# Optimization experiments

Measured on AMD Instinct MI355X. Metric: run time of the kernel, lower is better.

## Reference

```python
import jax, jax.numpy as jnp
import numpy as np

B, T, U = 4, 256, 128
EH, PH, JH, V = 1024, 640, 640, 1024


def setup_inputs() -> dict:
    key = jax.random.key(0)
    ks = jax.random.split(key, 8)
    s_e = 1.0 / np.sqrt(EH)
    s_p = 1.0 / np.sqrt(PH)
    s_j = 1.0 / np.sqrt(JH)
    return {
        "enc": jax.random.normal(ks[0], (B, EH, T), jnp.float32),
        "dec": jax.random.normal(ks[1], (B, PH, U), jnp.float32),
        "W_enc": jax.random.uniform(ks[2], (JH, EH), jnp.float32, -s_e, s_e),
        "b_enc": jax.random.uniform(ks[3], (JH,), jnp.float32, -s_e, s_e),
        "W_pred": jax.random.uniform(ks[4], (JH, PH), jnp.float32, -s_p, s_p),
        "b_pred": jax.random.uniform(ks[5], (JH,), jnp.float32, -s_p, s_p),
        "W_out": jax.random.uniform(ks[6], (V, JH), jnp.float32, -s_j, s_j),
        "b_out": jax.random.uniform(ks[7], (V,), jnp.float32, -s_j, s_j),
    }


def reference(enc, dec, W_enc, b_enc, W_pred, b_pred, W_out, b_out):
    # enc: [B, EH, T], dec: [B, PH, U]  (channels-first, as in torch forward)
    # enc projection -> [B, T, JH] (transpose fused into einsum)
    e = jnp.einsum('bht,jh->btj', enc, W_enc) + b_enc
    # pred projection -> [B, U, JH]
    p = jnp.einsum('bhu,jh->buj', dec, W_pred) + b_pred
    # broadcast add -> [B, T, U, JH], ReLU, output projection -> [B, T, U, V]
    h = jax.nn.relu(e[:, :, None, :] + p[:, None, :, :])
    logits = jnp.einsum('btuj,vj->btuv', h, W_out) + b_out
    return jax.nn.log_softmax(logits, axis=-1)
```

## Files before the change

### kernel.cpp

```cpp
#include <hip/hip_runtime.h>
#include <hip/hip_bf16.h>
#include <stdint.h>

#define B_ 4
#define T_ 256
#define U_ 128
#define EH_ 1024
#define PH_ 640
#define JH_ 640
#define V_ 1024
#define KT_ 20

typedef short bf16x8 __attribute__((ext_vector_type(8)));
typedef float f32x4 __attribute__((ext_vector_type(4)));
typedef unsigned short u16;

__device__ __forceinline__ u16 f2bf(float f) {
  union { float f; uint32_t u; } v;
  v.f = f;
  uint32_t u = v.u;
  return (u16)((u + 0x7FFFu + ((u >> 16) & 1u)) >> 16);
}

__device__ __forceinline__ uint32_t cvt2(float lo, float hi) {
  uint32_t r;
  asm("v_cvt_pk_bf16_f32 %0, %1, %2" : "=v"(r) : "v"(lo), "v"(hi));
  return r;
}

#define LGKM0  asm volatile("s_waitcnt lgkmcnt(0)" ::: "memory")

__global__ void k_transpose_cvt(const float* __restrict__ in, u16* __restrict__ out,
                                int H, int W) {
  __shared__ float tile[32][33];
  int b = blockIdx.z;
  int h0 = blockIdx.y * 32, w0 = blockIdx.x * 32;
  const float* pin = in + (size_t)b * H * W;
  u16* pout = out + (size_t)b * H * W;
  int lw = threadIdx.x & 31, lh = threadIdx.x >> 5;
#pragma unroll
  for (int i = 0; i < 4; i++) {
    int h = lh + i * 8;
    tile[h][lw] = pin[(size_t)(h0 + h) * W + (w0 + lw)];
  }
  __syncthreads();
#pragma unroll
  for (int i = 0; i < 4; i++) {
    int w = lh + i * 8;
    pout[(size_t)(w0 + w) * H + (h0 + lw)] = f2bf(tile[lw][w]);
  }
}

__global__ void k_prep_w(const float* __restrict__ We, const float* __restrict__ Wp,
                         const float* __restrict__ Wo,
                         u16* __restrict__ WeB, u16* __restrict__ WpB,
                         u16* __restrict__ Wpk) {
  int s = blockIdx.x * 256 + threadIdx.x;
  if (s < 163840) {
    int idx = s * 4;
    float4 v = *(const float4*)(We + idx);
    ushort4 o;
    o.x = f2bf(v.x); o.y = f2bf(v.y); o.z = f2bf(v.z); o.w = f2bf(v.w);
    *(ushort4*)(WeB + idx) = o;
  } else if (s < 266240) {
    int idx = (s - 163840) * 4;
    float4 v = *(const float4*)(Wp + idx);
    ushort4 o;
    o.x = f2bf(v.x); o.y = f2bf(v.y); o.z = f2bf(v.z); o.w = f2bf(v.w);
    *(ushort4*)(WpB + idx) = o;
  } else {
    int q = s - 266240;
    int c = q & 1023;
    int g = (q >> 10) & 3;
    int t = q >> 12;
    const float* src = Wo + (size_t)c * JH_ + t * 32 + g * 8;
    float4 a = *(const float4*)src;
    float4 b2 = *(const float4*)(src + 4);
    ushort4 lo, hi;
    lo.x = f2bf(a.x);  lo.y = f2bf(a.y);  lo.z = f2bf(a.z);  lo.w = f2bf(a.w);
    hi.x = f2bf(b2.x); hi.y = f2bf(b2.y); hi.z = f2bf(b2.z); hi.w = f2bf(b2.w);
    u16* d = Wpk + (size_t)q * 8;
    *(ushort4*)d = lo;
    *(ushort4*)(d + 4) = hi;
  }
}

__global__ void k_proj_gemm(const u16* __restrict__ A, const u16* __restrict__ Bm,
                            const float* __restrict__ bias, float* __restrict__ C,
                            int K, int N, size_t strideA, size_t strideC) {
  __shared__ __align__(16) u16 sA[64 * 64];
  __shared__ __align__(16) u16 sB[64 * 64];
  int bb = blockIdx.z;
  const u16* Ab = A + (size_t)bb * strideA;
  float* Cb = C + (size_t)bb * strideC;
  int m0 = blockIdx.x * 64, n0 = blockIdx.y * 64;
  int tid = threadIdx.x;
  int lane = tid & 63, wid = tid >> 6;

  f32x4 acc[2][2] = {};
  for (int kk = 0; kk < K; kk += 64) {
#pragma unroll
    for (int i = 0; i < 2; i++) {
      int c = tid + i * 256;
      int r = c >> 3, kc = c & 7;
      int s = (r << 3) | (kc ^ (r & 7));
      *(bf16x8*)(sA + s * 8) = *(const bf16x8*)(Ab + (size_t)(m0 + r) * K + kk + kc * 8);
      *(bf16x8*)(sB + s * 8) = *(const bf16x8*)(Bm + (size_t)(n0 + r) * K + kk + kc * 8);
    }
    __syncthreads();
    int wr = (wid >> 1) * 32, wc = (wid & 1) * 32;
    int lr = lane & 15, lk = lane >> 4;
#pragma unroll
    for (int ki = 0; ki < 2; ki++) {
      bf16x8 af[2], bq[2];
#pragma unroll
      for (int mf = 0; mf < 2; mf++) {
        int r = wr + mf * 16 + lr;
        int kc = ki * 4 + lk;
        int s = (r << 3) | (kc ^ (r & 7));
        af[mf] = *(const bf16x8*)(sA + s * 8);
      }
#pragma unroll
      for (int nf = 0; nf < 2; nf++) {
        int r = wc + nf * 16 + lr;
        int kc = ki * 4 + lk;
        int s = (r << 3) | (kc ^ (r & 7));
        bq[nf] = *(const bf16x8*)(sB + s * 8);
      }
#pragma unroll
      for (int mf = 0; mf < 2; mf++)
#pragma unroll
        for (int nf = 0; nf < 2; nf++)
          acc[mf][nf] = __builtin_amdgcn_mfma_f32_16x16x32_bf16(af[mf], bq[nf], acc[mf][nf], 0, 0, 0);
    }
    __syncthreads();
  }
  int wr = (wid >> 1) * 32, wc = (wid & 1) * 32;
  int lr = lane & 15, lq = lane >> 4;
#pragma unroll
  for (int nf = 0; nf < 2; nf++) {
    int n = n0 + wc + nf * 16 + lr;
    float bv = bias[n];
#pragma unroll
    for (int mf = 0; mf < 2; mf++) {
#pragma unroll
      for (int r = 0; r < 4; r++) {
        int m = m0 + wr + mf * 16 + lq * 4 + r;
        Cb[(size_t)m * N + n] = acc[mf][nf][r] + bv;
      }
    }
  }
}

__global__ void k_pack_p2(const float* __restrict__ pBuf, float* __restrict__ pPk) {
  int s = blockIdx.x * 256 + threadIdx.x;
  int bh = s / 10240;
  int rem = s - bh * 10240;
  int g4 = rem >> 6;
  int r = rem & 63;
  int b = bh >> 1, half = bh & 1;
  const float* src = pBuf + ((size_t)(b * 128 + half * 64 + r)) * JH_ + g4 * 4;
  float4 v = *(const float4*)src;
  *(float4*)(pPk + (size_t)s * 4) = v;
}

__global__ __launch_bounds__(512)
void k_fused4(const float* __restrict__ e, const float* __restrict__ pPk,
              const u16* __restrict__ Wpk, const float* __restrict__ bout,
              float* __restrict__ out) {
  __shared__ __align__(16) u16 sA[2][4096];
  __shared__ __align__(16) float sE[JH_];
  __shared__ float redm[512];
  __shared__ float reds[512];

  int bid = blockIdx.x;
  int btile = bid >> 1, half = bid & 1, b = btile >> 8;
  int tid = threadIdx.x, lane = tid & 63, wn = tid >> 6;
  int lr = lane & 15, lk = lane >> 4;
  int ph = (bid % 10) * 2;

  const float* eRow = e + (size_t)btile * JH_;
  const float* pPbase = pPk + ((size_t)(b * 2 + half) * 40960) + wn * 256 + lane * 4;
  const u16* wB = Wpk + ((size_t)lk * 1024 + wn * 128 + lr) * 8;
  float* outB = out + ((size_t)btile * U_ + half * 64) * V_;

  int awr = (wn >> 1) * 512 + lane * 8 + (wn & 1) * 4;

  f32x4 acc[4][8] = {};
  bf16x8 bq[2][8];

  auto tp = [&](int t) { int x = t + ph; return x >= KT_ ? x - KT_ : x; };
  auto loadB = [&](int tph, bf16x8* d) {
#pragma unroll
    for (int nf = 0; nf < 8; nf++)
      d[nf] = *(const bf16x8*)(wB + (size_t)tph * 32768 + nf * 128);
  };
  auto loadp = [&](int tph) { return *(const float4*)(pPbase + tph * 2048); };
  auto build = [&](int slot, int tin, int tph, float4 pv) {
    float4 ev = *(const float4*)(&sE[tph * 32 + wn * 4]);
    uint2 w;
    w.x = cvt2(fmaxf(pv.x + ev.x, 0.f), fmaxf(pv.y + ev.y, 0.f));
    w.y = cvt2(fmaxf(pv.z + ev.z, 0.f), fmaxf(pv.w + ev.w, 0.f));
    *(uint2*)(&sA[slot][tin * 2048 + awr]) = w;
  };

  loadB(tp(0), bq[0]);
  for (int i = tid; i < JH_; i += 512) sE[i] = eRow[i];
  float4 p0  = loadp(tp(0));
  float4 p1  = loadp(tp(1));
  float4 pcA = loadp(tp(2));
  float4 pcB = loadp(tp(3));
  float4 pnA = p0, pnB = p0;
  LGKM0;
  __builtin_amdgcn_s_barrier();
  build(0, 0, tp(0), p0);
  build(0, 1, tp(1), p1);
  LGKM0;
  __builtin_amdgcn_s_barrier();

#pragma unroll
  for (int t = 0; t < KT_; t++) {
    if (t + 1 < KT_) loadB(tp(t + 1), bq[(t + 1) & 1]);
    if ((t & 1) == 0) {
      if (t + 4 < KT_) { pnA = loadp(tp(t + 4)); pnB = loadp(tp(t + 5)); }
      if (t + 2 < KT_) {
        int q1 = ((t >> 1) + 1) & 1;
        build(q1, 0, tp(t + 2), pcA);
        build(q1, 1, tp(t + 3), pcB);
      }
    }
    const u16* Ab = &sA[(t >> 1) & 1][(t & 1) * 2048 + lk * 512];
    bf16x8 af[4];
#pragma unroll
    for (int mf = 0; mf < 4; mf++)
      af[mf] = *(const bf16x8*)(Ab + (mf * 16 + lr) * 8);
    __builtin_amdgcn_s_setprio(1);
#pragma unroll
    for (int mf = 0; mf < 4; mf++)
#pragma unroll
      for (int nf = 0; nf < 8; nf++)
        acc[mf][nf] = __builtin_amdgcn_mfma_f32_16x16x32_bf16(af[mf], bq[t & 1][nf], acc[mf][nf], 0, 0, 0);
    __builtin_amdgcn_s_setprio(0);
    if ((t & 1) && t + 1 < KT_) {
      pcA = pnA; pcB = pnB;
      LGKM0;
      __builtin_amdgcn_s_barrier();
    }
  }

  float bv[8];
#pragma unroll
  for (int nf = 0; nf < 8; nf++) bv[nf] = bout[wn * 128 + nf * 16 + lr];
#pragma unroll
  for (int mf = 0; mf < 4; mf++)
#pragma unroll
    for (int nf = 0; nf < 8; nf++)
#pragma unroll
      for (int r = 0; r < 4; r++)
        acc[mf][nf][r] += bv[nf];

  float gm[4][4];
#pragma unroll
  for (int mf = 0; mf < 4; mf++)
#pragma unroll
    for (int r = 0; r < 4; r++) {
      float m = acc[mf][0][r];
#pragma unroll
      for (int nf = 1; nf < 8; nf++) m = fmaxf(m, acc[mf][nf][r]);
#pragma unroll
      for (int o = 1; o < 16; o <<= 1) m = fmaxf(m, __shfl_xor(m, o, 64));
      gm[mf][r] = m;
    }
  if ((lane & 15) == 0) {
#pragma unroll
    for (int mf = 0; mf < 4; mf++)
#pragma unroll
      for (int r = 0; r < 4; r++)
        redm[(mf * 16 + lk * 4 + r) * 8 + wn] = gm[mf][r];
  }
  __syncthreads();
#pragma unroll
  for (int mf = 0; mf < 4; mf++)
#pragma unroll
    for (int r = 0; r < 4; r++) {
      int row = mf * 16 + lk * 4 + r;
      float m = redm[row * 8];
#pragma unroll
      for (int w = 1; w < 8; w++) m = fmaxf(m, redm[row * 8 + w]);
      gm[mf][r] = m;
    }
  float ls[4][4];
#pragma unroll
  for (int mf = 0; mf < 4; mf++)
#pragma unroll
    for (int r = 0; r < 4; r++) {
      float s = 0.f;
#pragma unroll
      for (int nf = 0; nf < 8; nf++) s += __expf(acc[mf][nf][r] - gm[mf][r]);
#pragma unroll
      for (int o = 1; o < 16; o <<= 1) s += __shfl_xor(s, o, 64);
      ls[mf][r] = s;
    }
  if ((lane & 15) == 0) {
#pragma unroll
    for (int mf = 0; mf < 4; mf++)
#pragma unroll
      for (int r = 0; r < 4; r++)
        reds[(mf * 16 + lk * 4 + r) * 8 + wn] = ls[mf][r];
  }
  __syncthreads();
#pragma unroll
  for (int mf = 0; mf < 4; mf++)
#pragma unroll
    for (int r = 0; r < 4; r++) {
      int row = mf * 16 + lk * 4 + r;
      float s = reds[row * 8];
#pragma unroll
      for (int w = 1; w < 8; w++) s += reds[row * 8 + w];
      ls[mf][r] = gm[mf][r] + __logf(s);
    }
#pragma unroll
  for (int mf = 0; mf < 4; mf++)
#pragma unroll
    for (int nf = 0; nf < 8; nf++)
#pragma unroll
      for (int r = 0; r < 4; r++)
        outB[(size_t)(mf * 16 + lk * 4 + r) * V_ + wn * 128 + nf * 16 + lr] =
            acc[mf][nf][r] - ls[mf][r];
}

extern "C" void kernel_launch(void* const* d_in, const int* in_sizes, int n_in,
                              void* d_out, int out_size, void* d_ws, size_t ws_size,
                              hipStream_t stream) {
  const float* enc    = (const float*)d_in[0];
  const float* dec    = (const float*)d_in[1];
  const float* W_enc  = (const float*)d_in[2];
  const float* b_enc  = (const float*)d_in[3];
  const float* W_pred = (const float*)d_in[4];
  const float* b_pred = (const float*)d_in[5];
  const float* W_out  = (const float*)d_in[6];
  const float* b_out  = (const float*)d_in[7];
  float* out = (float*)d_out;

  char* ws = (char*)d_ws;
  size_t off = 0;
  auto alloc = [&](size_t bytes) {
    void* pp = ws + off;
    off = (off + bytes + 255) & ~(size_t)255;
    return pp;
  };
  u16* encT   = (u16*)alloc((size_t)B_ * T_ * EH_ * 2);
  u16* decT   = (u16*)alloc((size_t)B_ * U_ * PH_ * 2);
  u16* WencB  = (u16*)alloc((size_t)JH_ * EH_ * 2);
  u16* WpredB = (u16*)alloc((size_t)JH_ * PH_ * 2);
  u16* Wpk    = (u16*)alloc((size_t)KT_ * 32768 * 2);
  float* eBuf = (float*)alloc((size_t)B_ * T_ * JH_ * 4);
  float* pBuf = (float*)alloc((size_t)B_ * U_ * JH_ * 4);
  float* pPk  = (float*)alloc((size_t)81920 * 4 * 4);

  k_transpose_cvt<<<dim3(T_ / 32, EH_ / 32, B_), 256, 0, stream>>>(enc, encT, EH_, T_);
  k_transpose_cvt<<<dim3(U_ / 32, PH_ / 32, B_), 256, 0, stream>>>(dec, decT, PH_, U_);
  k_prep_w<<<1360, 256, 0, stream>>>(W_enc, W_pred, W_out, WencB, WpredB, Wpk);
  k_proj_gemm<<<dim3(T_ / 64, JH_ / 64, B_), 256, 0, stream>>>(
      encT, WencB, b_enc, eBuf, EH_, JH_, (size_t)T_ * EH_, (size_t)T_ * JH_);
  k_proj_gemm<<<dim3(U_ / 64, JH_ / 64, B_), 256, 0, stream>>>(
      decT, WpredB, b_pred, pBuf, PH_, JH_, (size_t)U_ * PH_, (size_t)U_ * JH_);
  k_pack_p2<<<320, 256, 0, stream>>>(pBuf, pPk);

  k_fused4<<<B_ * T_ * 2, 512, 0, stream>>>(eBuf, pPk, Wpk, b_out, out);
}
```

Baseline: 298.9 us.

## Stage full pred tile in LDS as bf16 and build A fragments per wave

The fused joint kernel now loads the whole 64x640 pred slice into LDS as bf16 once at block start. Each wave then builds its own A fragments in registers (add enc row, ReLU, convert to bf16) from LDS, instead of cooperatively building a double-buffered shared A tile with a barrier every two k-steps. Per-wave k-phase staggering and launch bounds of two blocks per CU aim to cut barrier stalls and spread weight-load traffic. In exchange, each wave redoes the ReLU/convert work, LDS use grows to about 83 KB, and the pred values are rounded to bf16 before the add.

```diff
diff --git a/kernel.cpp b/kernel.cpp
--- a/kernel.cpp
+++ b/kernel.cpp
@@ -13,6 +13,7 @@
 
 typedef short bf16x8 __attribute__((ext_vector_type(8)));
 typedef float f32x4 __attribute__((ext_vector_type(4)));
+typedef uint32_t u32x4 __attribute__((ext_vector_type(4)));
 typedef unsigned short u16;
 
 __device__ __forceinline__ u16 f2bf(float f) {
@@ -28,7 +29,11 @@
   return r;
 }
 
-#define LGKM0  asm volatile("s_waitcnt lgkmcnt(0)" ::: "memory")
+__device__ __forceinline__ float asf(uint32_t u) {
+  union { uint32_t u; float f; } v;
+  v.u = u;
+  return v.f;
+}
 
 __global__ void k_transpose_cvt(const float* __restrict__ in, u16* __restrict__ out,
                                 int H, int W) {
@@ -164,11 +169,11 @@
   *(float4*)(pPk + (size_t)s * 4) = v;
 }
 
-__global__ __launch_bounds__(512)
-void k_fused4(const float* __restrict__ e, const float* __restrict__ pPk,
+__global__ __launch_bounds__(512, 2)
+void k_fused5(const float* __restrict__ e, const float* __restrict__ pPk,
               const u16* __restrict__ Wpk, const float* __restrict__ bout,
               float* __restrict__ out) {
-  __shared__ __align__(16) u16 sA[2][4096];
+  __shared__ __align__(16) u16 sP[64 * 648];
   __shared__ __align__(16) float sE[JH_];
   __shared__ float redm[512];
   __shared__ float reds[512];
@@ -177,75 +182,81 @@
   int btile = bid >> 1, half = bid & 1, b = btile >> 8;
   int tid = threadIdx.x, lane = tid & 63, wn = tid >> 6;
   int lr = lane & 15, lk = lane >> 4;
-  int ph = (bid % 10) * 2;
+  int phw = ((bid >> 3) * 7 + wn * 2) % KT_;
 
   const float* eRow = e + (size_t)btile * JH_;
-  const float* pPbase = pPk + ((size_t)(b * 2 + half) * 40960) + wn * 256 + lane * 4;
+  const float* pPbase = pPk + ((size_t)(b * 2 + half) * 40960);
   const u16* wB = Wpk + ((size_t)lk * 1024 + wn * 128 + lr) * 8;
   float* outB = out + ((size_t)btile * U_ + half * 64) * V_;
 
-  int awr = (wn >> 1) * 512 + lane * 8 + (wn & 1) * 4;
+  for (int i = tid; i < JH_; i += 512) sE[i] = eRow[i];
+#pragma unroll
+  for (int i = 0; i < 20; i++) {
+    int s = i * 512 + tid;
+    int r = s & 63, g4 = s >> 6;
+    float4 v = *(const float4*)(pPbase + (size_t)s * 4);
+    uint2 w2;
+    w2.x = cvt2(v.x, v.y);
+    w2.y = cvt2(v.z, v.w);
+    *(uint2*)(&sP[r * 648 + g4 * 4]) = w2;
+  }
+  __syncthreads();
 
   f32x4 acc[4][8] = {};
   bf16x8 bq[2][8];
-
-  auto tp = [&](int t) { int x = t + ph; return x >= KT_ ? x - KT_ : x; };
-  auto loadB = [&](int tph, bf16x8* d) {
+  u32x4 pd[2][4];
+  f32x4 ev[2][2];
+  bf16x8 af[4];
+
+  auto tpw = [&](int t) { int x = t + phw; return x >= KT_ ? x - KT_ : x; };
+  auto loadB = [&](int tw, bf16x8* d) {
 #pragma unroll
     for (int nf = 0; nf < 8; nf++)
-      d[nf] = *(const bf16x8*)(wB + (size_t)tph * 32768 + nf * 128);
+      d[nf] = *(const bf16x8*)(wB + (size_t)tw * 32768 + nf * 128);
   };
-  auto loadp = [&](int tph) { return *(const float4*)(pPbase + tph * 2048); };
-  auto build = [&](int slot, int tin, int tph, float4 pv) {
-    float4 ev = *(const float4*)(&sE[tph * 32 + wn * 4]);
-    uint2 w;
-    w.x = cvt2(fmaxf(pv.x + ev.x, 0.f), fmaxf(pv.y + ev.y, 0.f));
-    w.y = cvt2(fmaxf(pv.z + ev.z, 0.f), fmaxf(pv.w + ev.w, 0.f));
-    *(uint2*)(&sA[slot][tin * 2048 + awr]) = w;
+  auto loadA = [&](int tw, u32x4* pdv, f32x4* evv) {
+    int ko = tw * 32 + lk * 8;
+#pragma unroll
+    for (int mf = 0; mf < 4; mf++)
+      pdv[mf] = *(const u32x4*)(&sP[(mf * 16 + lr) * 648 + ko]);
+    evv[0] = *(const f32x4*)(&sE[ko]);
+    evv[1] = *(const f32x4*)(&sE[ko + 4]);
   };
-
-  loadB(tp(0), bq[0]);
-  for (int i = tid; i < JH_; i += 512) sE[i] = eRow[i];
-  float4 p0  = loadp(tp(0));
-  float4 p1  = loadp(tp(1));
-  float4 pcA = loadp(tp(2));
-  float4 pcB = loadp(tp(3));
-  float4 pnA = p0, pnB = p0;
-  LGKM0;
-  __builtin_amdgcn_s_barrier();
-  build(0, 0, tp(0), p0);
-  build(0, 1, tp(1), p1);
-  LGKM0;
-  __builtin_amdgcn_s_barrier();
+  auto build = [&](const u32x4* pdv, const f32x4* evv) {
+#pragma unroll
+    for (int mf = 0; mf < 4; mf++) {
+      union { uint32_t u[4]; bf16x8 v; } r;
+#pragma unroll
+      for (int j = 0; j < 4; j++) {
+        uint32_t u = pdv[mf][j];
+        float lo = asf(u << 16);
+        float hi = asf(u & 0xffff0000u);
+        float el = evv[j >> 1][(j & 1) * 2];
+        float eh = evv[j >> 1][(j & 1) * 2 + 1];
+        r.u[j] = cvt2(fmaxf(lo + el, 0.f), fmaxf(hi + eh, 0.f));
+      }
+      af[mf] = r.v;
+    }
+  };
+
+  loadA(tpw(0), pd[0], ev[0]);
+  loadB(tpw(0), bq[0]);
 
 #pragma unroll
   for (int t = 0; t < KT_; t++) {
-    if (t + 1 < KT_) loadB(tp(t + 1), bq[(t + 1) & 1]);
-    if ((t & 1) == 0) {
-      if (t + 4 < KT_) { pnA = loadp(tp(t + 4)); pnB = loadp(tp(t + 5)); }
-      if (t + 2 < KT_) {
-        int q1 = ((t >> 1) + 1) & 1;
-        build(q1, 0, tp(t + 2), pcA);
-        build(q1, 1, tp(t + 3), pcB);
-      }
-    }
-    const u16* Ab = &sA[(t >> 1) & 1][(t & 1) * 2048 + lk * 512];
-    bf16x8 af[4];
+    const int c = t & 1;
+    if (t + 1 < KT_) {
+      loadA(tpw(t + 1), pd[c ^ 1], ev[c ^ 1]);
+      loadB(tpw(t + 1), bq[c ^ 1]);
+    }
+    build(pd[c], ev[c]);
+    __builtin_amdgcn_s_setprio(1);
 #pragma unroll
     for (int mf = 0; mf < 4; mf++)
-      af[mf] = *(const bf16x8*)(Ab + (mf * 16 + lr) * 8);
-    __builtin_amdgcn_s_setprio(1);
-#pragma unroll
-    for (int mf = 0; mf < 4; mf++)
 #pragma unroll
       for (int nf = 0; nf < 8; nf++)
-        acc[mf][nf] = __builtin_amdgcn_mfma_f32_16x16x32_bf16(af[mf], bq[t & 1][nf], acc[mf][nf], 0, 0, 0);
+        acc[mf][nf] = __builtin_amdgcn_mfma_f32_16x16x32_bf16(af[mf], bq[c][nf], acc[mf][nf], 0, 0, 0);
     __builtin_amdgcn_s_setprio(0);
-    if ((t & 1) && t + 1 < KT_) {
-      pcA = pnA; pcB = pnB;
-      LGKM0;
-      __builtin_amdgcn_s_barrier();
-    }
   }
 
   float bv[8];
@@ -367,5 +378,5 @@
       decT, WpredB, b_pred, pBuf, PH_, JH_, (size_t)U_ * PH_, (size_t)U_ * JH_);
   k_pack_p2<<<320, 256, 0, stream>>>(pBuf, pPk);
 
-  k_fused4<<<B_ * T_ * 2, 512, 0, stream>>>(eBuf, pPk, Wpk, b_out, out);
-}
+  k_fused5<<<B_ * T_ * 2, 512, 0, stream>>>(eBuf, pPk, Wpk, b_out, out);
+}
```

Result: slower. 329.3 us (+10.2%).

## Make fused joint kernel persistent and transpose MFMA operands for vector stores

Applied to the files above, without the earlier changes.

Launches 256 persistent blocks, each looping over 8 (t, half) units instead of one block per unit, and prefetches the next unit's e row, W and p fragments while the current unit's output is written. Swaps the MFMA operand order so each lane holds four consecutive vocabulary columns. This allows 16-byte vectorized output stores and bias loads, and cuts the softmax shuffle reductions to two steps per row. The cost is fewer resident blocks, so latency hiding depends on the in-block prefetch. The sE overwrite in stageUnit also relies on barrier ordering being correct.

```diff
diff --git a/kernel.cpp b/kernel.cpp
--- a/kernel.cpp
+++ b/kernel.cpp
@@ -165,7 +165,7 @@
 }
 
 __global__ __launch_bounds__(512)
-void k_fused4(const float* __restrict__ e, const float* __restrict__ pPk,
+void k_fused6(const float* __restrict__ e, const float* __restrict__ pPk,
               const u16* __restrict__ Wpk, const float* __restrict__ bout,
               float* __restrict__ out) {
   __shared__ __align__(16) u16 sA[2][4096];
@@ -174,20 +174,17 @@
   __shared__ float reds[512];
 
   int bid = blockIdx.x;
-  int btile = bid >> 1, half = bid & 1, b = btile >> 8;
   int tid = threadIdx.x, lane = tid & 63, wn = tid >> 6;
   int lr = lane & 15, lk = lane >> 4;
   int ph = (bid % 10) * 2;
 
-  const float* eRow = e + (size_t)btile * JH_;
-  const float* pPbase = pPk + ((size_t)(b * 2 + half) * 40960) + wn * 256 + lane * 4;
   const u16* wB = Wpk + ((size_t)lk * 1024 + wn * 128 + lr) * 8;
-  float* outB = out + ((size_t)btile * U_ + half * 64) * V_;
-
   int awr = (wn >> 1) * 512 + lane * 8 + (wn & 1) * 4;
 
-  f32x4 acc[4][8] = {};
   bf16x8 bq[2][8];
+  float4 p0, p1, pcA, pcB, pnA, pnB;
+  const float* pPbase = pPk;
+  float* outB = out;
 
   auto tp = [&](int t) { int x = t + ph; return x >= KT_ ? x - KT_ : x; };
   auto loadB = [&](int tph, bf16x8* d) {
@@ -203,130 +200,128 @@
     w.y = cvt2(fmaxf(pv.z + ev.z, 0.f), fmaxf(pv.w + ev.w, 0.f));
     *(uint2*)(&sA[slot][tin * 2048 + awr]) = w;
   };
-
-  loadB(tp(0), bq[0]);
-  for (int i = tid; i < JH_; i += 512) sE[i] = eRow[i];
-  float4 p0  = loadp(tp(0));
-  float4 p1  = loadp(tp(1));
-  float4 pcA = loadp(tp(2));
-  float4 pcB = loadp(tp(3));
-  float4 pnA = p0, pnB = p0;
-  LGKM0;
-  __builtin_amdgcn_s_barrier();
-  build(0, 0, tp(0), p0);
-  build(0, 1, tp(1), p1);
-  LGKM0;
-  __builtin_amdgcn_s_barrier();
-
-#pragma unroll
-  for (int t = 0; t < KT_; t++) {
-    if (t + 1 < KT_) loadB(tp(t + 1), bq[(t + 1) & 1]);
-    if ((t & 1) == 0) {
-      if (t + 4 < KT_) { pnA = loadp(tp(t + 4)); pnB = loadp(tp(t + 5)); }
-      if (t + 2 < KT_) {
-        int q1 = ((t >> 1) + 1) & 1;
-        build(q1, 0, tp(t + 2), pcA);
-        build(q1, 1, tp(t + 3), pcB);
-      }
-    }
-    const u16* Ab = &sA[(t >> 1) & 1][(t & 1) * 2048 + lk * 512];
-    bf16x8 af[4];
-#pragma unroll
-    for (int mf = 0; mf < 4; mf++)
-      af[mf] = *(const bf16x8*)(Ab + (mf * 16 + lr) * 8);
-    __builtin_amdgcn_s_setprio(1);
-#pragma unroll
-    for (int mf = 0; mf < 4; mf++)
+  auto stageUnit = [&](int unit) {
+    int btile = unit >> 1, half = unit & 1, b = btile >> 8;
+    const float* eRow = e + (size_t)btile * JH_;
+    pPbase = pPk + ((size_t)(b * 2 + half) * 40960) + wn * 256 + lane * 4;
+    outB = out + ((size_t)btile * U_ + half * 64) * V_;
+    for (int i = tid; i < JH_; i += 512) sE[i] = eRow[i];
+    loadB(tp(0), bq[0]);
+    p0  = loadp(tp(0));
+    p1  = loadp(tp(1));
+    pcA = loadp(tp(2));
+    pcB = loadp(tp(3));
+  };
+
+  stageUnit(bid);
+
+#pragma unroll 1
+  for (int u = 0; u < 8; u++) {
+    LGKM0;
+    __builtin_amdgcn_s_barrier();
+    build(0, 0, tp(0), p0);
+    build(0, 1, tp(1), p1);
+    LGKM0;
+    __builtin_amdgcn_s_barrier();
+
+    f32x4 acc[4][8] = {};
+#pragma unroll
+    for (int t = 0; t < KT_; t++) {
+      if (t + 1 < KT_) loadB(tp(t + 1), bq[(t + 1) & 1]);
+      if ((t & 1) == 0) {
+        if (t + 4 < KT_) { pnA = loadp(tp(t + 4)); pnB = loadp(tp(t + 5)); }
+        if (t + 2 < KT_) {
+          int q1 = ((t >> 1) + 1) & 1;
+          build(q1, 0, tp(t + 2), pcA);
+          build(q1, 1, tp(t + 3), pcB);
+        }
+      }
+      const u16* Ab = &sA[(t >> 1) & 1][(t & 1) * 2048 + lk * 512];
+      bf16x8 af[4];
+#pragma unroll
+      for (int mf = 0; mf < 4; mf++)
+        af[mf] = *(const bf16x8*)(Ab + (mf * 16 + lr) * 8);
+      __builtin_amdgcn_s_setprio(1);
+#pragma unroll
+      for (int mf = 0; mf < 4; mf++)
+#pragma unroll
+        for (int nf = 0; nf < 8; nf++)
+          acc[mf][nf] = __builtin_amdgcn_mfma_f32_16x16x32_bf16(bq[t & 1][nf], af[mf], acc[mf][nf], 0, 0, 0);
+      __builtin_amdgcn_s_setprio(0);
+      if ((t & 1) && t + 1 < KT_) {
+        pcA = pnA; pcB = pnB;
+        LGKM0;
+        __builtin_amdgcn_s_barrier();
+      }
+    }
+
+#pragma unroll
+    for (int nf = 0; nf < 8; nf++) {
+      f32x4 bv = *(const f32x4*)(bout + wn * 128 + nf * 16 + lk * 4);
+#pragma unroll
+      for (int mf = 0; mf < 4; mf++) acc[mf][nf] += bv;
+    }
+    float gm[4], lsv[4];
+#pragma unroll
+    for (int mf = 0; mf < 4; mf++) {
+      float m = acc[mf][0][0];
 #pragma unroll
       for (int nf = 0; nf < 8; nf++)
-        acc[mf][nf] = __builtin_amdgcn_mfma_f32_16x16x32_bf16(af[mf], bq[t & 1][nf], acc[mf][nf], 0, 0, 0);
-    __builtin_amdgcn_s_setprio(0);
-    if ((t & 1) && t + 1 < KT_) {
-      pcA = pnA; pcB = pnB;
-      LGKM0;
-      __builtin_amdgcn_s_barrier();
-    }
-  }
-
-  float bv[8];
-#pragma unroll
-  for (int nf = 0; nf < 8; nf++) bv[nf] = bout[wn * 128 + nf * 16 + lr];
-#pragma unroll
-  for (int mf = 0; mf < 4; mf++)
-#pragma unroll
-    for (int nf = 0; nf < 8; nf++)
-#pragma unroll
-      for (int r = 0; r < 4; r++)
-        acc[mf][nf][r] += bv[nf];
-
-  float gm[4][4];
-#pragma unroll
-  for (int mf = 0; mf < 4; mf++)
-#pragma unroll
-    for (int r = 0; r < 4; r++) {
-      float m = acc[mf][0][r];
-#pragma unroll
-      for (int nf = 1; nf < 8; nf++) m = fmaxf(m, acc[mf][nf][r]);
-#pragma unroll
-      for (int o = 1; o < 16; o <<= 1) m = fmaxf(m, __shfl_xor(m, o, 64));
-      gm[mf][r] = m;
-    }
-  if ((lane & 15) == 0) {
-#pragma unroll
-    for (int mf = 0; mf < 4; mf++)
-#pragma unroll
-      for (int r = 0; r < 4; r++)
-        redm[(mf * 16 + lk * 4 + r) * 8 + wn] = gm[mf][r];
-  }
-  __syncthreads();
-#pragma unroll
-  for (int mf = 0; mf < 4; mf++)
-#pragma unroll
-    for (int r = 0; r < 4; r++) {
-      int row = mf * 16 + lk * 4 + r;
-      float m = redm[row * 8];
-#pragma unroll
-      for (int w = 1; w < 8; w++) m = fmaxf(m, redm[row * 8 + w]);
-      gm[mf][r] = m;
-    }
-  float ls[4][4];
-#pragma unroll
-  for (int mf = 0; mf < 4; mf++)
-#pragma unroll
-    for (int r = 0; r < 4; r++) {
+#pragma unroll
+        for (int j = 0; j < 4; j++) m = fmaxf(m, acc[mf][nf][j]);
+      m = fmaxf(m, __shfl_xor(m, 16, 64));
+      m = fmaxf(m, __shfl_xor(m, 32, 64));
+      gm[mf] = m;
+    }
+    if (lane < 16) {
+#pragma unroll
+      for (int mf = 0; mf < 4; mf++) redm[(mf * 16 + lr) * 8 + wn] = gm[mf];
+    }
+    __syncthreads();
+#pragma unroll
+    for (int mf = 0; mf < 4; mf++) {
+      float m = redm[(mf * 16 + lr) * 8];
+#pragma unroll
+      for (int w = 1; w < 8; w++) m = fmaxf(m, redm[(mf * 16 + lr) * 8 + w]);
+      gm[mf] = m;
+    }
+#pragma unroll
+    for (int mf = 0; mf < 4; mf++) {
       float s = 0.f;
 #pragma unroll
-      for (int nf = 0; nf < 8; nf++) s += __expf(acc[mf][nf][r] - gm[mf][r]);
-#pragma unroll
-      for (int o = 1; o < 16; o <<= 1) s += __shfl_xor(s, o, 64);
-      ls[mf][r] = s;
-    }
-  if ((lane & 15) == 0) {
-#pragma unroll
-    for (int mf = 0; mf < 4; mf++)
-#pragma unroll
-      for (int r = 0; r < 4; r++)
-        reds[(mf * 16 + lk * 4 + r) * 8 + wn] = ls[mf][r];
-  }
-  __syncthreads();
-#pragma unroll
-  for (int mf = 0; mf < 4; mf++)
-#pragma unroll
-    for (int r = 0; r < 4; r++) {
-      int row = mf * 16 + lk * 4 + r;
-      float s = reds[row * 8];
-#pragma unroll
-      for (int w = 1; w < 8; w++) s += reds[row * 8 + w];
-      ls[mf][r] = gm[mf][r] + __logf(s);
-    }
-#pragma unroll
-  for (int mf = 0; mf < 4; mf++)
-#pragma unroll
-    for (int nf = 0; nf < 8; nf++)
-#pragma unroll
-      for (int r = 0; r < 4; r++)
-        outB[(size_t)(mf * 16 + lk * 4 + r) * V_ + wn * 128 + nf * 16 + lr] =
-            acc[mf][nf][r] - ls[mf][r];
+      for (int nf = 0; nf < 8; nf++)
+#pragma unroll
+        for (int j = 0; j < 4; j++) s += __expf(acc[mf][nf][j] - gm[mf]);
+      s += __shfl_xor(s, 16, 64);
+      s += __shfl_xor(s, 32, 64);
+      lsv[mf] = s;
+    }
+    if (lane < 16) {
+#pragma unroll
+      for (int mf = 0; mf < 4; mf++) reds[(mf * 16 + lr) * 8 + wn] = lsv[mf];
+    }
+    __syncthreads();
+#pragma unroll
+    for (int mf = 0; mf < 4; mf++) {
+      float s = reds[(mf * 16 + lr) * 8];
+#pragma unroll
+      for (int w = 1; w < 8; w++) s += reds[(mf * 16 + lr) * 8 + w];
+      lsv[mf] = gm[mf] + __logf(s);
+    }
+
+    float* outC = outB;
+    if (u < 7) stageUnit((u + 1) * 256 + bid);
+
+#pragma unroll
+    for (int mf = 0; mf < 4; mf++) {
+      float* orow = outC + (size_t)(mf * 16 + lr) * V_ + wn * 128 + lk * 4;
+#pragma unroll
+      for (int nf = 0; nf < 8; nf++) {
+        f32x4 v = acc[mf][nf] - lsv[mf];
+        *(f32x4*)(orow + nf * 16) = v;
+      }
+    }
+  }
 }
 
 extern "C" void kernel_launch(void* const* d_in, const int* in_sizes, int n_in,
@@ -367,5 +362,5 @@
       decT, WpredB, b_pred, pBuf, PH_, JH_, (size_t)U_ * PH_, (size_t)U_ * JH_);
   k_pack_p2<<<320, 256, 0, stream>>>(pBuf, pPk);
 
-  k_fused4<<<B_ * T_ * 2, 512, 0, stream>>>(eBuf, pPk, Wpk, b_out, out);
-}
+  k_fused6<<<256, 512, 0, stream>>>(eBuf, pPk, Wpk, b_out, out);
+}
```

New measurement: 392.7 us. 31.4% more time.
